# Kernel optimization log

Hardware: AMD Instinct MI355X
Metric: run time of the kernel (lower is better)

## Reference

```python
import jax, jax.numpy as jnp
import numpy as np
from jax import lax

D = 1024      # input_dim
H = 4096      # hidden_dim (4*D)
E = 8         # num_experts
TOPK = 2      # sparse_top_k


def setup_inputs() -> dict:
    key = jax.random.key(0)
    ks = jax.random.split(key, 7)
    s = 0.02
    return {
        "x": jax.random.normal(ks[0], (2, 2048, D), dtype=jnp.float32),
        "W1": jax.random.normal(ks[1], (E, D, H), dtype=jnp.float32) * s,
        "b1": jnp.zeros((E, H), dtype=jnp.float32),
        "W2": jax.random.normal(ks[2], (E, H, D), dtype=jnp.float32) * s,
        "b2": jnp.zeros((E, D), dtype=jnp.float32),
        "Wr": jax.random.normal(ks[3], (D, E), dtype=jnp.float32) * s,
        "br": jnp.zeros((E,), dtype=jnp.float32),
    }


def reference(x, W1, b1, W2, b2, Wr, br):
    B, S, _ = x.shape
    xf = x.reshape(-1, D)                                  # [T, D]
    logits = xf @ Wr + br                                  # [T, E]
    # top-k threshold masking (keep logits >= k-th largest, else -inf)
    topv, _ = lax.top_k(logits, TOPK)                      # [T, k]
    thresh = topv[:, TOPK - 1:TOPK]                        # [T, 1]
    masked = jnp.where(logits >= thresh, logits, -jnp.inf)
    weights = jax.nn.softmax(masked, axis=-1)              # [T, E]
    # run ALL experts densely (faithful to reference), then weighted sum
    h = jax.nn.gelu(jnp.einsum('td,edh->eth', xf, W1) + b1[:, None, :],
                    approximate=False)                     # [E, T, H]
    expert_out = jnp.einsum('eth,ehd->etd', h, W2) + b2[:, None, :]  # [E, T, D]
    out = jnp.einsum('etd,te->td', expert_out, weights)    # [T, D]
    return out.reshape(B, S, D)
```

## Files before the change

### kernel.cpp

```cpp
#include <hip/hip_runtime.h>
#include <math.h>

typedef __bf16 bf16x8 __attribute__((ext_vector_type(8)));
typedef float f32x4 __attribute__((ext_vector_type(4)));

#define DDIM 1024
#define HDIM 4096
#define NE 8
#define TT 4096
#define CAP 9216

static const size_t OFF_CTRL   = 0;
static const size_t OFF_ROWMAP = 256;
static const size_t OFF_WROW   = OFF_ROWMAP + (size_t)CAP * 4;
static const size_t OFF_ROWPOS = OFF_WROW + (size_t)CAP * 4;
static const size_t OFF_TOKE   = OFF_ROWPOS + (size_t)TT * 2 * 4;
static const size_t OFF_TOKW   = OFF_TOKE + (size_t)TT * 2 * 4;
static const size_t OFF_XB     = OFF_TOKW + (size_t)TT * 2 * 4;
static const size_t OFF_W1T    = OFF_XB + (size_t)TT * DDIM * 2;
static const size_t OFF_W2T    = OFF_W1T + (size_t)NE * HDIM * DDIM * 2;
static const size_t OFF_H      = OFF_W2T + (size_t)NE * DDIM * HDIM * 2;
static const size_t OFF_PO     = OFF_H + (size_t)CAP * HDIM * 2;
static const size_t WS_NEED    = OFF_PO + (size_t)CAP * DDIM * 2;

__device__ __forceinline__ unsigned short f2bf(float f) {
  unsigned int u = __builtin_bit_cast(unsigned int, f);
  u = (u + 0x7FFFu + ((u >> 16) & 1u)) >> 16;
  return (unsigned short)u;
}

__device__ __forceinline__ float bf2f(unsigned short s) {
  return __builtin_bit_cast(float, (unsigned int)s << 16);
}

__device__ __forceinline__ void async16(void* lds, const void* g) {
  __builtin_amdgcn_global_load_lds(
      (__attribute__((address_space(1))) void*)g,
      (__attribute__((address_space(3))) void*)lds, 16, 0, 0);
}

__device__ __forceinline__ float gelu_exact(float v) {
  return 0.5f * v * (1.0f + erff(v * 0.70710678118654752f));
}

__global__ __launch_bounds__(256) void router_k(
    const float* __restrict__ x, const float* __restrict__ Wr, const float* __restrict__ br,
    unsigned short* __restrict__ xb, int* __restrict__ toke, float* __restrict__ tokw) {
  int tid = threadIdx.x, lane = tid & 63, wid = tid >> 6;
  int t = blockIdx.x * 4 + wid;
  const float* xr = x + (size_t)t * DDIM;
  float acc[NE];
#pragma unroll
  for (int e = 0; e < NE; ++e) acc[e] = 0.f;
#pragma unroll
  for (int it = 0; it < DDIM / 256; ++it) {
    int d0 = it * 256 + lane * 4;
    float4 xv = *(const float4*)(xr + d0);
    ushort4 xs;
    xs.x = f2bf(xv.x); xs.y = f2bf(xv.y); xs.z = f2bf(xv.z); xs.w = f2bf(xv.w);
    *(ushort4*)(xb + (size_t)t * DDIM + d0) = xs;
    const float4* w0 = (const float4*)(Wr + (size_t)(d0 + 0) * NE);
    const float4* w1 = (const float4*)(Wr + (size_t)(d0 + 1) * NE);
    const float4* w2 = (const float4*)(Wr + (size_t)(d0 + 2) * NE);
    const float4* w3 = (const float4*)(Wr + (size_t)(d0 + 3) * NE);
    float4 a, b;
    a = w0[0]; b = w0[1];
    acc[0] += xv.x * a.x; acc[1] += xv.x * a.y; acc[2] += xv.x * a.z; acc[3] += xv.x * a.w;
    acc[4] += xv.x * b.x; acc[5] += xv.x * b.y; acc[6] += xv.x * b.z; acc[7] += xv.x * b.w;
    a = w1[0]; b = w1[1];
    acc[0] += xv.y * a.x; acc[1] += xv.y * a.y; acc[2] += xv.y * a.z; acc[3] += xv.y * a.w;
    acc[4] += xv.y * b.x; acc[5] += xv.y * b.y; acc[6] += xv.y * b.z; acc[7] += xv.y * b.w;
    a = w2[0]; b = w2[1];
    acc[0] += xv.z * a.x; acc[1] += xv.z * a.y; acc[2] += xv.z * a.z; acc[3] += xv.z * a.w;
    acc[4] += xv.z * b.x; acc[5] += xv.z * b.y; acc[6] += xv.z * b.z; acc[7] += xv.z * b.w;
    a = w3[0]; b = w3[1];
    acc[0] += xv.w * a.x; acc[1] += xv.w * a.y; acc[2] += xv.w * a.z; acc[3] += xv.w * a.w;
    acc[4] += xv.w * b.x; acc[5] += xv.w * b.y; acc[6] += xv.w * b.z; acc[7] += xv.w * b.w;
  }
#pragma unroll
  for (int e = 0; e < NE; ++e) {
#pragma unroll
    for (int s = 32; s > 0; s >>= 1) acc[e] += __shfl_xor(acc[e], s, 64);
  }
  if (lane == 0) {
    float l[NE];
#pragma unroll
    for (int e = 0; e < NE; ++e) l[e] = acc[e] + br[e];
    int i0 = 0; float m0 = l[0];
#pragma unroll
    for (int e = 1; e < NE; ++e) if (l[e] > m0) { m0 = l[e]; i0 = e; }
    int i1 = -1; float m1 = -3.4e38f;
#pragma unroll
    for (int e = 0; e < NE; ++e) if (e != i0 && l[e] > m1) { m1 = l[e]; i1 = e; }
    float e1 = expf(m1 - m0);
    float s = 1.f + e1;
    toke[2 * t] = i0;  toke[2 * t + 1] = i1;
    tokw[2 * t] = 1.f / s;  tokw[2 * t + 1] = e1 / s;
  }
}

__global__ __launch_bounds__(1024) void bin_k(
    const int* __restrict__ toke, const float* __restrict__ tokw,
    int* __restrict__ ctrl, int* __restrict__ rowmap,
    float* __restrict__ wrow, int* __restrict__ rowpos) {
  __shared__ int wcnt[16][8];
  __shared__ int wpre[16][8];
  __shared__ int pbase[9];
  __shared__ int ecnt[8];
  __shared__ int ebase[8];
  int tid = threadIdx.x, lane = tid & 63, w = tid >> 6;

  int myCnt = 0;
  for (int c = 0; c < 8; ++c) {
    int e = toke[c * 1024 + tid];
#pragma unroll
    for (int ee = 0; ee < 8; ++ee) {
      unsigned long long m = __ballot(e == ee);
      if (lane == ee) myCnt += (int)__popcll(m);
    }
  }
  if (lane < 8) wcnt[w][lane] = myCnt;
  __syncthreads();
  if (tid == 0) {
    int off = 0;
    for (int e = 0; e < 8; ++e) {
      int s = 0;
      for (int ww = 0; ww < 16; ++ww) s += wcnt[ww][e];
      ecnt[e] = s;
      pbase[e] = off;
      ebase[e] = off;
      ctrl[8 + e] = off;
      off += ((s + 127) >> 7) << 7;
    }
    pbase[8] = off;
    ctrl[16] = off;
  }
  __syncthreads();

  for (int e = 0; e < 8; ++e) {
    int start = pbase[e] + ecnt[e], end = pbase[e + 1];
    for (int r = start + tid; r < end; r += 1024) { rowmap[r] = 0; wrow[r] = 0.f; }
  }

  for (int c = 0; c < 8; ++c) {
    int slot = c * 1024 + tid;
    int e = toke[slot];
    unsigned long long mown = 0;
#pragma unroll
    for (int ee = 0; ee < 8; ++ee) {
      unsigned long long m = __ballot(e == ee);
      if (lane == ee) wcnt[w][ee] = (int)__popcll(m);
      if (e == ee) mown = m;
    }
    __syncthreads();
    if (tid < 128) {
      int ww = tid >> 3, ee = tid & 7;
      int s = 0;
      for (int p = 0; p < ww; ++p) s += wcnt[p][ee];
      wpre[ww][ee] = s;
    }
    __syncthreads();
    int rank = (int)__popcll(mown & ((1ull << lane) - 1ull));
    int r = ebase[e] + wpre[w][e] + rank;
    rowmap[r] = slot >> 1;
    wrow[r] = tokw[slot];
    rowpos[slot] = r;
    __syncthreads();
    if (tid < 8) {
      int s = 0;
      for (int ww = 0; ww < 16; ++ww) s += wcnt[ww][tid];
      ebase[tid] += s;
    }
    __syncthreads();
  }
}

__global__ __launch_bounds__(256) void convT_k(
    const float* __restrict__ src, unsigned short* __restrict__ dst, int K_, int N_) {
  __shared__ unsigned int lds32[64][33];
  int e = blockIdx.z;
  int kb = blockIdx.y << 6, nb = blockIdx.x << 6;
  int t = threadIdx.x;
  const float* s = src + (size_t)e * K_ * N_ + (size_t)kb * N_ + nb;
  int n0 = (t & 15) << 2;
#pragma unroll
  for (int i = 0; i < 2; ++i) {
    int k2 = (i << 4) + (t >> 4);
    float4 a = *(const float4*)(s + (size_t)(2 * k2) * N_ + n0);
    float4 b = *(const float4*)(s + (size_t)(2 * k2 + 1) * N_ + n0);
    lds32[n0 + 0][k2] = (unsigned)f2bf(a.x) | ((unsigned)f2bf(b.x) << 16);
    lds32[n0 + 1][k2] = (unsigned)f2bf(a.y) | ((unsigned)f2bf(b.y) << 16);
    lds32[n0 + 2][k2] = (unsigned)f2bf(a.z) | ((unsigned)f2bf(b.z) << 16);
    lds32[n0 + 3][k2] = (unsigned)f2bf(a.w) | ((unsigned)f2bf(b.w) << 16);
  }
  __syncthreads();
  unsigned short* dp = dst + (size_t)e * (size_t)N_ * K_ + (size_t)nb * K_ + kb;
  int n = t >> 2, c = t & 3;
  uint4 v0, v1;
  v0.x = lds32[n][(c << 2) + 0]; v0.y = lds32[n][(c << 2) + 1];
  v0.z = lds32[n][(c << 2) + 2]; v0.w = lds32[n][(c << 2) + 3];
  int c4 = (c + 4) << 2;
  v1.x = lds32[n][c4 + 0]; v1.y = lds32[n][c4 + 1];
  v1.z = lds32[n][c4 + 2]; v1.w = lds32[n][c4 + 3];
  *(uint4*)(dp + (size_t)n * K_ + (c << 3)) = v0;
  *(uint4*)(dp + (size_t)n * K_ + ((c + 4) << 3)) = v1;
}

template <int KTOT, int NTOT, bool GATHER, bool DOGELU, bool KSPLIT2>
__global__ __launch_bounds__(256, 2) void gemm_k(
    const unsigned short* __restrict__ A, const unsigned short* __restrict__ Bt,
    const int* __restrict__ ctrl, const int* __restrict__ rowmap,
    const float* __restrict__ wrow, const float* __restrict__ bias,
    unsigned short* __restrict__ out0, unsigned short* __restrict__ out1) {
  __shared__ __align__(16) char SMEM[32768];
  unsigned short* Asm = (unsigned short*)SMEM;
  unsigned short* Bsm = (unsigned short*)(SMEM + 16384);
  int zz = blockIdx.z;
  int e = KSPLIT2 ? (zz & 7) : zz;
  int ks = KSPLIT2 ? (zz >> 3) : 0;
  int off0 = ctrl[8 + e], off1 = ctrl[8 + e + 1];
  int row0 = off0 + (blockIdx.y << 7);
  if (row0 >= off1) return;
  int col0 = blockIdx.x << 7;
  int tid = threadIdx.x, lane = tid & 63, wid = tid >> 6;
  int wr = wid >> 1, wc = wid & 1;
  int kbeg = KSPLIT2 ? ks * (KTOT / 2) : 0;
  int kend = KSPLIT2 ? kbeg + (KTOT / 2) : KTOT;
  unsigned short* outp = (KSPLIT2 && ks) ? out1 : out0;
  if (DOGELU) outp = out0;

  const unsigned short* Asrc[4];
  const unsigned short* Bsrc[4];
#pragma unroll
  for (int c = 0; c < 4; ++c) {
    int ar = row0 + (c << 5) + (tid >> 3);
    size_t arow = GATHER ? (size_t)rowmap[ar] : (size_t)ar;
    Asrc[c] = A + arow * KTOT + ((tid & 7) << 3);
    int brw = col0 + (c << 5) + (tid >> 3);
    Bsrc[c] = Bt + ((size_t)e * NTOT + brw) * KTOT + ((tid & 7) << 3);
  }

  f32x4 acc[4][4];
#pragma unroll
  for (int m = 0; m < 4; ++m)
#pragma unroll
    for (int n = 0; n < 4; ++n) acc[m][n] = (f32x4){0.f, 0.f, 0.f, 0.f};

  int arow_rd = ((wr << 6) + (lane & 15)) << 6;
  int brow_rd = ((wc << 6) + (lane & 15)) << 6;
  int koff = (lane >> 4) << 3;

  for (int k0 = kbeg; k0 < kend; k0 += 64) {
#pragma unroll
    for (int c = 0; c < 4; ++c) {
      async16(SMEM + (((c << 8) + (wid << 6)) << 4), Asrc[c] + k0);
      async16(SMEM + 16384 + (((c << 8) + (wid << 6)) << 4), Bsrc[c] + k0);
    }
    __syncthreads();
#pragma unroll
    for (int kk = 0; kk < 64; kk += 32) {
      bf16x8 af[4], bfr[4];
#pragma unroll
      for (int m = 0; m < 4; ++m)
        af[m] = *(const bf16x8*)&Asm[arow_rd + (m << 10) + kk + koff];
#pragma unroll
      for (int n = 0; n < 4; ++n)
        bfr[n] = *(const bf16x8*)&Bsm[brow_rd + (n << 10) + kk + koff];
#pragma unroll
      for (int m = 0; m < 4; ++m)
#pragma unroll
        for (int n = 0; n < 4; ++n)
          acc[m][n] = __builtin_amdgcn_mfma_f32_16x16x32_bf16(af[m], bfr[n], acc[m][n], 0, 0, 0);
    }
    __syncthreads();
  }

  unsigned short (*Cl)[128] = (unsigned short(*)[128])SMEM;
  int r_b = (lane >> 4) << 2;
  int c_b = lane & 15;
#pragma unroll
  for (int n = 0; n < 4; ++n) {
    int col_l = (wc << 6) + (n << 4) + c_b;
    float bv = (KSPLIT2 && ks) ? 0.f : bias[e * NTOT + col0 + col_l];
#pragma unroll
    for (int m = 0; m < 4; ++m) {
#pragma unroll
      for (int r = 0; r < 4; ++r) {
        int row_l = (wr << 6) + (m << 4) + r_b + r;
        float v = acc[m][n][r] + bv;
        if (DOGELU) {
          Cl[row_l][col_l] = f2bf(gelu_exact(v));
        } else {
          Cl[row_l][col_l] = f2bf(wrow[row0 + row_l] * v);
        }
      }
    }
  }
  __syncthreads();
  int rb = tid >> 4, cof = (tid & 15) << 3;
#pragma unroll
  for (int j = 0; j < 8; ++j) {
    int row_l = rb + (j << 4);
    uint4 v = *(const uint4*)&Cl[row_l][cof];
    *(uint4*)&outp[(size_t)(row0 + row_l) * NTOT + col0 + cof] = v;
  }
}

__global__ __launch_bounds__(256) void gather_k(
    const unsigned short* __restrict__ p0, const unsigned short* __restrict__ p1,
    const int* __restrict__ rowpos, float* __restrict__ out) {
  int t = blockIdx.x, d = threadIdx.x << 2;
  int r0 = rowpos[2 * t], r1 = rowpos[2 * t + 1];
  ushort4 a0 = *(const ushort4*)&p0[(size_t)r0 * DDIM + d];
  ushort4 a1 = *(const ushort4*)&p1[(size_t)r0 * DDIM + d];
  ushort4 b0 = *(const ushort4*)&p0[(size_t)r1 * DDIM + d];
  ushort4 b1 = *(const ushort4*)&p1[(size_t)r1 * DDIM + d];
  float4 o;
  o.x = (bf2f(a0.x) + bf2f(a1.x)) + (bf2f(b0.x) + bf2f(b1.x));
  o.y = (bf2f(a0.y) + bf2f(a1.y)) + (bf2f(b0.y) + bf2f(b1.y));
  o.z = (bf2f(a0.z) + bf2f(a1.z)) + (bf2f(b0.z) + bf2f(b1.z));
  o.w = (bf2f(a0.w) + bf2f(a1.w)) + (bf2f(b0.w) + bf2f(b1.w));
  *(float4*)&out[(size_t)t * DDIM + d] = o;
}

extern "C" void kernel_launch(void* const* d_in, const int* in_sizes, int n_in,
                              void* d_out, int out_size, void* d_ws, size_t ws_size,
                              hipStream_t stream) {
  const float* x  = (const float*)d_in[0];
  const float* W1 = (const float*)d_in[1];
  const float* b1 = (const float*)d_in[2];
  const float* W2 = (const float*)d_in[3];
  const float* b2 = (const float*)d_in[4];
  const float* Wr = (const float*)d_in[5];
  const float* br = (const float*)d_in[6];
  float* out = (float*)d_out;

  if (ws_size < WS_NEED) return;

  char* ws = (char*)d_ws;
  int* ctrl            = (int*)(ws + OFF_CTRL);
  int* rowmap          = (int*)(ws + OFF_ROWMAP);
  float* wrow          = (float*)(ws + OFF_WROW);
  int* rowpos          = (int*)(ws + OFF_ROWPOS);
  int* toke            = (int*)(ws + OFF_TOKE);
  float* tokw          = (float*)(ws + OFF_TOKW);
  unsigned short* xb   = (unsigned short*)(ws + OFF_XB);
  unsigned short* W1T  = (unsigned short*)(ws + OFF_W1T);
  unsigned short* W2T  = (unsigned short*)(ws + OFF_W2T);
  unsigned short* hbuf = (unsigned short*)(ws + OFF_H);
  unsigned short* pout = (unsigned short*)(ws + OFF_PO);
  unsigned short* pout2 = (unsigned short*)(ws + OFF_W1T);

  router_k<<<TT / 4, 256, 0, stream>>>(x, Wr, br, xb, toke, tokw);
  bin_k<<<1, 1024, 0, stream>>>(toke, tokw, ctrl, rowmap, wrow, rowpos);

  convT_k<<<dim3(HDIM / 64, DDIM / 64, NE), 256, 0, stream>>>(W1, W1T, DDIM, HDIM);
  convT_k<<<dim3(DDIM / 64, HDIM / 64, NE), 256, 0, stream>>>(W2, W2T, HDIM, DDIM);

  gemm_k<DDIM, HDIM, true, true, false><<<dim3(HDIM / 128, 32, NE), 256, 0, stream>>>(
      xb, W1T, ctrl, rowmap, wrow, b1, hbuf, nullptr);
  gemm_k<HDIM, DDIM, false, false, true><<<dim3(DDIM / 128, 32, NE * 2), 256, 0, stream>>>(
      hbuf, W2T, ctrl, rowmap, wrow, b2, pout, pout2);

  gather_k<<<TT, 256, 0, stream>>>(pout, pout2, rowpos, out);
}
```

Before: 374.6 us.

## Widen GEMM block tile to 128x256 for more operand reuse

The expert GEMM kernel moves from a 128x128 to a 128x256 output tile per block. Each wave now computes 64x128 with 32 accumulator fragments, and shared memory grows to 48KB to stage the wider B tile. The epilogue is split into four 64-column quarters that go through a smaller LDS staging buffer with extra barriers. The aim is to cut global and LDS traffic per MFMA by reusing A fragments across twice as many columns. The cost is higher register pressure under launch_bounds(256,2), and half as many blocks, which may hurt occupancy and load balance on the many CUs.

```diff
diff --git a/kernel.cpp b/kernel.cpp
--- a/kernel.cpp
+++ b/kernel.cpp
@@ -206,13 +206,13 @@
   *(uint4*)(dp + (size_t)n * K_ + ((c + 4) << 3)) = v1;
 }
 
-template <int KTOT, int NTOT, bool GATHER, bool DOGELU, bool KSPLIT2>
+template <int KTOT, int KLEN, int NTOT, bool GATHER, bool DOGELU, bool KSPLIT2>
 __global__ __launch_bounds__(256, 2) void gemm_k(
     const unsigned short* __restrict__ A, const unsigned short* __restrict__ Bt,
     const int* __restrict__ ctrl, const int* __restrict__ rowmap,
     const float* __restrict__ wrow, const float* __restrict__ bias,
     unsigned short* __restrict__ out0, unsigned short* __restrict__ out1) {
-  __shared__ __align__(16) char SMEM[32768];
+  __shared__ __align__(16) char SMEM[49152];
   unsigned short* Asm = (unsigned short*)SMEM;
   unsigned short* Bsm = (unsigned short*)(SMEM + 16384);
   int zz = blockIdx.z;
@@ -221,88 +221,107 @@
   int off0 = ctrl[8 + e], off1 = ctrl[8 + e + 1];
   int row0 = off0 + (blockIdx.y << 7);
   if (row0 >= off1) return;
-  int col0 = blockIdx.x << 7;
-  int tid = threadIdx.x, lane = tid & 63, wid = tid >> 6;
+  int col0 = blockIdx.x << 8;
+  int tid = threadIdx.x, lane = tid & 63;
+  int wid = tid >> 6;
   int wr = wid >> 1, wc = wid & 1;
-  int kbeg = KSPLIT2 ? ks * (KTOT / 2) : 0;
-  int kend = KSPLIT2 ? kbeg + (KTOT / 2) : KTOT;
+  int kbeg = KSPLIT2 ? ks * KLEN : 0;
   unsigned short* outp = (KSPLIT2 && ks) ? out1 : out0;
   if (DOGELU) outp = out0;
 
   const unsigned short* Asrc[4];
-  const unsigned short* Bsrc[4];
+  const unsigned short* Bsrc[8];
 #pragma unroll
   for (int c = 0; c < 4; ++c) {
     int ar = row0 + (c << 5) + (tid >> 3);
     size_t arow = GATHER ? (size_t)rowmap[ar] : (size_t)ar;
-    Asrc[c] = A + arow * KTOT + ((tid & 7) << 3);
+    Asrc[c] = A + arow * KTOT + kbeg + ((tid & 7) << 3);
+  }
+#pragma unroll
+  for (int c = 0; c < 8; ++c) {
     int brw = col0 + (c << 5) + (tid >> 3);
-    Bsrc[c] = Bt + ((size_t)e * NTOT + brw) * KTOT + ((tid & 7) << 3);
-  }
-
-  f32x4 acc[4][4];
+    Bsrc[c] = Bt + ((size_t)e * NTOT + brw) * KTOT + kbeg + ((tid & 7) << 3);
+  }
+
+  f32x4 acc[4][8];
 #pragma unroll
   for (int m = 0; m < 4; ++m)
 #pragma unroll
-    for (int n = 0; n < 4; ++n) acc[m][n] = (f32x4){0.f, 0.f, 0.f, 0.f};
-
-  int arow_rd = ((wr << 6) + (lane & 15)) << 6;
-  int brow_rd = ((wc << 6) + (lane & 15)) << 6;
+    for (int n = 0; n < 8; ++n) acc[m][n] = (f32x4){0.f, 0.f, 0.f, 0.f};
+
+  int rA[4], rB[8];
+#pragma unroll
+  for (int m = 0; m < 4; ++m) rA[m] = ((wr << 6) + (m << 4) + (lane & 15)) << 6;
+#pragma unroll
+  for (int n = 0; n < 8; ++n) rB[n] = ((wc << 7) + (n << 4) + (lane & 15)) << 6;
   int koff = (lane >> 4) << 3;
 
-  for (int k0 = kbeg; k0 < kend; k0 += 64) {
-#pragma unroll
-    for (int c = 0; c < 4; ++c) {
-      async16(SMEM + (((c << 8) + (wid << 6)) << 4), Asrc[c] + k0);
-      async16(SMEM + 16384 + (((c << 8) + (wid << 6)) << 4), Bsrc[c] + k0);
-    }
+  for (int k0 = 0; k0 < KLEN; k0 += 64) {
+#pragma unroll
+    for (int c = 0; c < 4; ++c)
+      async16(SMEM + c * 4096 + tid * 16, Asrc[c] + k0);
+#pragma unroll
+    for (int c = 0; c < 8; ++c)
+      async16(SMEM + 16384 + c * 4096 + tid * 16, Bsrc[c] + k0);
     __syncthreads();
 #pragma unroll
     for (int kk = 0; kk < 64; kk += 32) {
-      bf16x8 af[4], bfr[4];
+      bf16x8 af[4];
 #pragma unroll
       for (int m = 0; m < 4; ++m)
-        af[m] = *(const bf16x8*)&Asm[arow_rd + (m << 10) + kk + koff];
-#pragma unroll
-      for (int n = 0; n < 4; ++n)
-        bfr[n] = *(const bf16x8*)&Bsm[brow_rd + (n << 10) + kk + koff];
-#pragma unroll
-      for (int m = 0; m < 4; ++m)
+        af[m] = *(const bf16x8*)&Asm[rA[m] + kk + koff];
+#pragma unroll
+      for (int g = 0; g < 2; ++g) {
+        bf16x8 bfr[4];
 #pragma unroll
         for (int n = 0; n < 4; ++n)
-          acc[m][n] = __builtin_amdgcn_mfma_f32_16x16x32_bf16(af[m], bfr[n], acc[m][n], 0, 0, 0);
-    }
-    __syncthreads();
-  }
-
-  unsigned short (*Cl)[128] = (unsigned short(*)[128])SMEM;
+          bfr[n] = *(const bf16x8*)&Bsm[rB[(g << 2) + n] + kk + koff];
+#pragma unroll
+        for (int m = 0; m < 4; ++m)
+#pragma unroll
+          for (int n = 0; n < 4; ++n)
+            acc[m][(g << 2) + n] =
+                __builtin_amdgcn_mfma_f32_16x16x32_bf16(af[m], bfr[n], acc[m][(g << 2) + n], 0, 0, 0);
+      }
+    }
+    __syncthreads();
+  }
+
+  unsigned short (*Cl)[64] = (unsigned short(*)[64])SMEM;
   int r_b = (lane >> 4) << 2;
   int c_b = lane & 15;
 #pragma unroll
-  for (int n = 0; n < 4; ++n) {
-    int col_l = (wc << 6) + (n << 4) + c_b;
-    float bv = (KSPLIT2 && ks) ? 0.f : bias[e * NTOT + col0 + col_l];
-#pragma unroll
-    for (int m = 0; m < 4; ++m) {
-#pragma unroll
-      for (int r = 0; r < 4; ++r) {
-        int row_l = (wr << 6) + (m << 4) + r_b + r;
-        float v = acc[m][n][r] + bv;
-        if (DOGELU) {
-          Cl[row_l][col_l] = f2bf(gelu_exact(v));
-        } else {
-          Cl[row_l][col_l] = f2bf(wrow[row0 + row_l] * v);
+  for (int q = 0; q < 4; ++q) {
+    if (wc == (q >> 1)) {
+#pragma unroll
+      for (int nn = 0; nn < 4; ++nn) {
+        int n = ((q & 1) << 2) + nn;
+        int col_q = (nn << 4) + c_b;
+        float bv = (KSPLIT2 && ks) ? 0.f : bias[e * NTOT + col0 + (q << 6) + col_q];
+#pragma unroll
+        for (int m = 0; m < 4; ++m) {
+#pragma unroll
+          for (int r = 0; r < 4; ++r) {
+            int row_l = (wr << 6) + (m << 4) + r_b + r;
+            float v = acc[m][n][r] + bv;
+            if (DOGELU) {
+              Cl[row_l][col_q] = f2bf(gelu_exact(v));
+            } else {
+              Cl[row_l][col_q] = f2bf(wrow[row0 + row_l] * v);
+            }
+          }
         }
       }
     }
-  }
-  __syncthreads();
-  int rb = tid >> 4, cof = (tid & 15) << 3;
-#pragma unroll
-  for (int j = 0; j < 8; ++j) {
-    int row_l = rb + (j << 4);
-    uint4 v = *(const uint4*)&Cl[row_l][cof];
-    *(uint4*)&outp[(size_t)(row0 + row_l) * NTOT + col0 + cof] = v;
+    __syncthreads();
+    int rb = tid >> 3, cof = (tid & 7) << 3;
+#pragma unroll
+    for (int j = 0; j < 4; ++j) {
+      int row_l = rb + (j << 5);
+      uint4 v = *(const uint4*)&Cl[row_l][cof];
+      *(uint4*)&outp[(size_t)(row0 + row_l) * NTOT + col0 + (q << 6) + cof] = v;
+    }
+    __syncthreads();
   }
 }
 
@@ -357,9 +376,9 @@
   convT_k<<<dim3(HDIM / 64, DDIM / 64, NE), 256, 0, stream>>>(W1, W1T, DDIM, HDIM);
   convT_k<<<dim3(DDIM / 64, HDIM / 64, NE), 256, 0, stream>>>(W2, W2T, HDIM, DDIM);
 
-  gemm_k<DDIM, HDIM, true, true, false><<<dim3(HDIM / 128, 32, NE), 256, 0, stream>>>(
+  gemm_k<DDIM, DDIM, HDIM, true, true, false><<<dim3(HDIM / 256, 32, NE), 256, 0, stream>>>(
       xb, W1T, ctrl, rowmap, wrow, b1, hbuf, nullptr);
-  gemm_k<HDIM, DDIM, false, false, true><<<dim3(DDIM / 128, 32, NE * 2), 256, 0, stream>>>(
+  gemm_k<HDIM, HDIM / 2, DDIM, false, false, true><<<dim3(DDIM / 256, 32, NE * 2), 256, 0, stream>>>(
       hbuf, W2T, ctrl, rowmap, wrow, b2, pout, pout2);
 
   gather_k<<<TT, 256, 0, stream>>>(pout, pout2, rowpos, out);
```

Result: slower. 465.6 us (+24.3%).

## Enlarge GEMM tiles to 256x128 with 512-thread blocks and 8 waves

Applied to the files above, without the earlier changes.

The expert GEMM kernel moves from 128x128 tiles with 4 waves to 256x128 tiles with 8 waves (4 along M, 2 along N). Each B tile loaded into LDS is now reused across twice as many rows, cutting weight traffic per FLOP. The epilogue writes the output in two 128-row halves through LDS, with row clamping and bounds checks for partial tiles, since padding per expert no longer aligns with 256. Risks are more LDS per block (48KB), lower occupancy, and more wasted work on ragged expert segments.

```diff
diff --git a/kernel.cpp b/kernel.cpp
--- a/kernel.cpp
+++ b/kernel.cpp
@@ -206,38 +206,41 @@
   *(uint4*)(dp + (size_t)n * K_ + ((c + 4) << 3)) = v1;
 }
 
-template <int KTOT, int NTOT, bool GATHER, bool DOGELU, bool KSPLIT2>
-__global__ __launch_bounds__(256, 2) void gemm_k(
+template <int KTOT, int KLEN, int NTOT, bool GATHER, bool DOGELU, bool KSPLIT2>
+__global__ __launch_bounds__(512, 2) void gemm_k(
     const unsigned short* __restrict__ A, const unsigned short* __restrict__ Bt,
     const int* __restrict__ ctrl, const int* __restrict__ rowmap,
     const float* __restrict__ wrow, const float* __restrict__ bias,
     unsigned short* __restrict__ out0, unsigned short* __restrict__ out1) {
-  __shared__ __align__(16) char SMEM[32768];
+  __shared__ __align__(16) char SMEM[49152];
   unsigned short* Asm = (unsigned short*)SMEM;
-  unsigned short* Bsm = (unsigned short*)(SMEM + 16384);
+  unsigned short* Bsm = (unsigned short*)(SMEM + 32768);
   int zz = blockIdx.z;
   int e = KSPLIT2 ? (zz & 7) : zz;
   int ks = KSPLIT2 ? (zz >> 3) : 0;
   int off0 = ctrl[8 + e], off1 = ctrl[8 + e + 1];
-  int row0 = off0 + (blockIdx.y << 7);
+  int row0 = off0 + (blockIdx.y << 8);
   if (row0 >= off1) return;
   int col0 = blockIdx.x << 7;
   int tid = threadIdx.x, lane = tid & 63, wid = tid >> 6;
-  int wr = wid >> 1, wc = wid & 1;
-  int kbeg = KSPLIT2 ? ks * (KTOT / 2) : 0;
-  int kend = KSPLIT2 ? kbeg + (KTOT / 2) : KTOT;
+  int wm = wid & 3, wn = wid >> 2;
+  int kbeg = KSPLIT2 ? ks * KLEN : 0;
   unsigned short* outp = (KSPLIT2 && ks) ? out1 : out0;
   if (DOGELU) outp = out0;
 
   const unsigned short* Asrc[4];
-  const unsigned short* Bsrc[4];
+  const unsigned short* Bsrc[2];
 #pragma unroll
   for (int c = 0; c < 4; ++c) {
-    int ar = row0 + (c << 5) + (tid >> 3);
+    int ar = row0 + (c << 6) + (tid >> 3);
+    if (ar > off1 - 1) ar = off1 - 1;
     size_t arow = GATHER ? (size_t)rowmap[ar] : (size_t)ar;
-    Asrc[c] = A + arow * KTOT + ((tid & 7) << 3);
-    int brw = col0 + (c << 5) + (tid >> 3);
-    Bsrc[c] = Bt + ((size_t)e * NTOT + brw) * KTOT + ((tid & 7) << 3);
+    Asrc[c] = A + arow * KTOT + kbeg + ((tid & 7) << 3);
+  }
+#pragma unroll
+  for (int c = 0; c < 2; ++c) {
+    int brw = col0 + (c << 6) + (tid >> 3);
+    Bsrc[c] = Bt + ((size_t)e * NTOT + brw) * KTOT + kbeg + ((tid & 7) << 3);
   }
 
   f32x4 acc[4][4];
@@ -246,26 +249,28 @@
 #pragma unroll
     for (int n = 0; n < 4; ++n) acc[m][n] = (f32x4){0.f, 0.f, 0.f, 0.f};
 
-  int arow_rd = ((wr << 6) + (lane & 15)) << 6;
-  int brow_rd = ((wc << 6) + (lane & 15)) << 6;
+  int rA[4], rB[4];
+#pragma unroll
+  for (int m = 0; m < 4; ++m) rA[m] = ((wm << 6) + (m << 4) + (lane & 15)) << 6;
+#pragma unroll
+  for (int n = 0; n < 4; ++n) rB[n] = ((wn << 6) + (n << 4) + (lane & 15)) << 6;
   int koff = (lane >> 4) << 3;
 
-  for (int k0 = kbeg; k0 < kend; k0 += 64) {
-#pragma unroll
-    for (int c = 0; c < 4; ++c) {
-      async16(SMEM + (((c << 8) + (wid << 6)) << 4), Asrc[c] + k0);
-      async16(SMEM + 16384 + (((c << 8) + (wid << 6)) << 4), Bsrc[c] + k0);
-    }
+  for (int k0 = 0; k0 < KLEN; k0 += 64) {
+#pragma unroll
+    for (int c = 0; c < 4; ++c)
+      async16(SMEM + (c << 13) + (tid << 4), Asrc[c] + k0);
+#pragma unroll
+    for (int c = 0; c < 2; ++c)
+      async16(SMEM + 32768 + (c << 13) + (tid << 4), Bsrc[c] + k0);
     __syncthreads();
 #pragma unroll
     for (int kk = 0; kk < 64; kk += 32) {
       bf16x8 af[4], bfr[4];
 #pragma unroll
-      for (int m = 0; m < 4; ++m)
-        af[m] = *(const bf16x8*)&Asm[arow_rd + (m << 10) + kk + koff];
-#pragma unroll
-      for (int n = 0; n < 4; ++n)
-        bfr[n] = *(const bf16x8*)&Bsm[brow_rd + (n << 10) + kk + koff];
+      for (int m = 0; m < 4; ++m) af[m] = *(const bf16x8*)&Asm[rA[m] + kk + koff];
+#pragma unroll
+      for (int n = 0; n < 4; ++n) bfr[n] = *(const bf16x8*)&Bsm[rB[n] + kk + koff];
 #pragma unroll
       for (int m = 0; m < 4; ++m)
 #pragma unroll
@@ -278,31 +283,46 @@
   unsigned short (*Cl)[128] = (unsigned short(*)[128])SMEM;
   int r_b = (lane >> 4) << 2;
   int c_b = lane & 15;
-#pragma unroll
-  for (int n = 0; n < 4; ++n) {
-    int col_l = (wc << 6) + (n << 4) + c_b;
-    float bv = (KSPLIT2 && ks) ? 0.f : bias[e * NTOT + col0 + col_l];
-#pragma unroll
-    for (int m = 0; m < 4; ++m) {
-#pragma unroll
-      for (int r = 0; r < 4; ++r) {
-        int row_l = (wr << 6) + (m << 4) + r_b + r;
-        float v = acc[m][n][r] + bv;
-        if (DOGELU) {
-          Cl[row_l][col_l] = f2bf(gelu_exact(v));
-        } else {
-          Cl[row_l][col_l] = f2bf(wrow[row0 + row_l] * v);
+  float bv[4];
+#pragma unroll
+  for (int n = 0; n < 4; ++n)
+    bv[n] = (KSPLIT2 && ks) ? 0.f : bias[e * NTOT + col0 + (wn << 6) + (n << 4) + c_b];
+
+#pragma unroll
+  for (int p = 0; p < 2; ++p) {
+    if ((wm >> 1) == p) {
+#pragma unroll
+      for (int n = 0; n < 4; ++n) {
+        int col_l = (wn << 6) + (n << 4) + c_b;
+#pragma unroll
+        for (int m = 0; m < 4; ++m) {
+#pragma unroll
+          for (int r = 0; r < 4; ++r) {
+            int row_l = ((wm & 1) << 6) + (m << 4) + r_b + r;
+            float v = acc[m][n][r] + bv[n];
+            if (DOGELU) {
+              Cl[row_l][col_l] = f2bf(gelu_exact(v));
+            } else {
+              int grow = row0 + (p << 7) + row_l;
+              int rw = grow < off1 ? grow : off0;
+              Cl[row_l][col_l] = f2bf(wrow[rw] * v);
+            }
+          }
         }
       }
     }
-  }
-  __syncthreads();
-  int rb = tid >> 4, cof = (tid & 15) << 3;
-#pragma unroll
-  for (int j = 0; j < 8; ++j) {
-    int row_l = rb + (j << 4);
-    uint4 v = *(const uint4*)&Cl[row_l][cof];
-    *(uint4*)&outp[(size_t)(row0 + row_l) * NTOT + col0 + cof] = v;
+    __syncthreads();
+    int rb = tid >> 4, cof = (tid & 15) << 3;
+#pragma unroll
+    for (int j = 0; j < 4; ++j) {
+      int row_l = rb + (j << 5);
+      int grow = row0 + (p << 7) + row_l;
+      if (grow < off1) {
+        uint4 v = *(const uint4*)&Cl[row_l][cof];
+        *(uint4*)&outp[(size_t)grow * NTOT + col0 + cof] = v;
+      }
+    }
+    __syncthreads();
   }
 }
 
@@ -357,9 +377,11 @@
   convT_k<<<dim3(HDIM / 64, DDIM / 64, NE), 256, 0, stream>>>(W1, W1T, DDIM, HDIM);
   convT_k<<<dim3(DDIM / 64, HDIM / 64, NE), 256, 0, stream>>>(W2, W2T, HDIM, DDIM);
 
-  gemm_k<DDIM, HDIM, true, true, false><<<dim3(HDIM / 128, 32, NE), 256, 0, stream>>>(
+  gemm_k<DDIM, DDIM, HDIM, true, true, false>
+      <<<dim3(HDIM / 128, 16, NE), 512, 0, stream>>>(
       xb, W1T, ctrl, rowmap, wrow, b1, hbuf, nullptr);
-  gemm_k<HDIM, DDIM, false, false, true><<<dim3(DDIM / 128, 32, NE * 2), 256, 0, stream>>>(
+  gemm_k<HDIM, HDIM / 2, DDIM, false, false, true>
+      <<<dim3(DDIM / 128, 16, NE * 2), 512, 0, stream>>>(
       hbuf, W2T, ctrl, rowmap, wrow, b2, pout, pout2);
 
   gather_k<<<TT, 256, 0, stream>>>(pout, pout2, rowpos, out);
```

Result: slower. 438.4 us (+17.0%).

## Co-schedule weight transposes with router and first GEMM in fused launches

Applied to the files above, without the earlier changes.

The W1 fp32-to-bf16 transpose is folded into the router kernel, interleaving eight transpose blocks per router block. The W2 transpose is folded into the first expert GEMM by alternating odd blocks (transpose) and even blocks (GEMM tiles). The aim is to overlap the memory-bound weight conversion with compute-bound GEMM work and to drop separate launches. The cost is heterogeneous blocks within one grid. The 32KB shared allocation applies to the transpose blocks too, which may lower occupancy, and many GEMM blocks exit early, which may leave scheduling uneven.

```diff
diff --git a/kernel.cpp b/kernel.cpp
--- a/kernel.cpp
+++ b/kernel.cpp
@@ -43,11 +43,52 @@
   return 0.5f * v * (1.0f + erff(v * 0.70710678118654752f));
 }
 
-__global__ __launch_bounds__(256) void router_k(
+__device__ __forceinline__ void convT_body(
+    const float* __restrict__ src, unsigned short* __restrict__ dst,
+    int K_, int N_, int e, int kbt, int nbt, char* smem) {
+  unsigned int (*lds32)[33] = (unsigned int(*)[33])smem;
+  int kb = kbt << 6, nb = nbt << 6;
+  int t = threadIdx.x;
+  const float* s = src + (size_t)e * K_ * N_ + (size_t)kb * N_ + nb;
+  int n0 = (t & 15) << 2;
+#pragma unroll
+  for (int i = 0; i < 2; ++i) {
+    int k2 = (i << 4) + (t >> 4);
+    float4 a = *(const float4*)(s + (size_t)(2 * k2) * N_ + n0);
+    float4 b = *(const float4*)(s + (size_t)(2 * k2 + 1) * N_ + n0);
+    lds32[n0 + 0][k2] = (unsigned)f2bf(a.x) | ((unsigned)f2bf(b.x) << 16);
+    lds32[n0 + 1][k2] = (unsigned)f2bf(a.y) | ((unsigned)f2bf(b.y) << 16);
+    lds32[n0 + 2][k2] = (unsigned)f2bf(a.z) | ((unsigned)f2bf(b.z) << 16);
+    lds32[n0 + 3][k2] = (unsigned)f2bf(a.w) | ((unsigned)f2bf(b.w) << 16);
+  }
+  __syncthreads();
+  unsigned short* dp = dst + (size_t)e * (size_t)N_ * K_ + (size_t)nb * K_ + kb;
+  int n = t >> 2, c = t & 3;
+  uint4 v0, v1;
+  v0.x = lds32[n][(c << 2) + 0]; v0.y = lds32[n][(c << 2) + 1];
+  v0.z = lds32[n][(c << 2) + 2]; v0.w = lds32[n][(c << 2) + 3];
+  int c4 = (c + 4) << 2;
+  v1.x = lds32[n][c4 + 0]; v1.y = lds32[n][c4 + 1];
+  v1.z = lds32[n][c4 + 2]; v1.w = lds32[n][c4 + 3];
+  *(uint4*)(dp + (size_t)n * K_ + (c << 3)) = v0;
+  *(uint4*)(dp + (size_t)n * K_ + ((c + 4) << 3)) = v1;
+}
+
+__global__ __launch_bounds__(256) void fat1_k(
     const float* __restrict__ x, const float* __restrict__ Wr, const float* __restrict__ br,
-    unsigned short* __restrict__ xb, int* __restrict__ toke, float* __restrict__ tokw) {
+    unsigned short* __restrict__ xb, int* __restrict__ toke, float* __restrict__ tokw,
+    const float* __restrict__ W1, unsigned short* __restrict__ W1T) {
+  __shared__ __align__(16) char SMEM[8448];
+  int b = blockIdx.x;
+  int g = b / 9, r = b % 9;
+  if (r != 0) {
+    int idx = 8 * g + (r - 1);
+    int e = idx >> 10, rem = idx & 1023;
+    convT_body(W1, W1T, DDIM, HDIM, e, rem >> 6, rem & 63, SMEM);
+    return;
+  }
   int tid = threadIdx.x, lane = tid & 63, wid = tid >> 6;
-  int t = blockIdx.x * 4 + wid;
+  int t = g * 4 + wid;
   const float* xr = x + (size_t)t * DDIM;
   float acc[NE];
 #pragma unroll
@@ -63,19 +104,19 @@
     const float4* w1 = (const float4*)(Wr + (size_t)(d0 + 1) * NE);
     const float4* w2 = (const float4*)(Wr + (size_t)(d0 + 2) * NE);
     const float4* w3 = (const float4*)(Wr + (size_t)(d0 + 3) * NE);
-    float4 a, b;
-    a = w0[0]; b = w0[1];
+    float4 a, bb;
+    a = w0[0]; bb = w0[1];
     acc[0] += xv.x * a.x; acc[1] += xv.x * a.y; acc[2] += xv.x * a.z; acc[3] += xv.x * a.w;
-    acc[4] += xv.x * b.x; acc[5] += xv.x * b.y; acc[6] += xv.x * b.z; acc[7] += xv.x * b.w;
-    a = w1[0]; b = w1[1];
+    acc[4] += xv.x * bb.x; acc[5] += xv.x * bb.y; acc[6] += xv.x * bb.z; acc[7] += xv.x * bb.w;
+    a = w1[0]; bb = w1[1];
     acc[0] += xv.y * a.x; acc[1] += xv.y * a.y; acc[2] += xv.y * a.z; acc[3] += xv.y * a.w;
-    acc[4] += xv.y * b.x; acc[5] += xv.y * b.y; acc[6] += xv.y * b.z; acc[7] += xv.y * b.w;
-    a = w2[0]; b = w2[1];
+    acc[4] += xv.y * bb.x; acc[5] += xv.y * bb.y; acc[6] += xv.y * bb.z; acc[7] += xv.y * bb.w;
+    a = w2[0]; bb = w2[1];
     acc[0] += xv.z * a.x; acc[1] += xv.z * a.y; acc[2] += xv.z * a.z; acc[3] += xv.z * a.w;
-    acc[4] += xv.z * b.x; acc[5] += xv.z * b.y; acc[6] += xv.z * b.z; acc[7] += xv.z * b.w;
-    a = w3[0]; b = w3[1];
+    acc[4] += xv.z * bb.x; acc[5] += xv.z * bb.y; acc[6] += xv.z * bb.z; acc[7] += xv.z * bb.w;
+    a = w3[0]; bb = w3[1];
     acc[0] += xv.w * a.x; acc[1] += xv.w * a.y; acc[2] += xv.w * a.z; acc[3] += xv.w * a.w;
-    acc[4] += xv.w * b.x; acc[5] += xv.w * b.y; acc[6] += xv.w * b.z; acc[7] += xv.w * b.w;
+    acc[4] += xv.w * bb.x; acc[5] += xv.w * bb.y; acc[6] += xv.w * bb.z; acc[7] += xv.w * bb.w;
   }
 #pragma unroll
   for (int e = 0; e < NE; ++e) {
@@ -175,67 +216,128 @@
   }
 }
 
-__global__ __launch_bounds__(256) void convT_k(
-    const float* __restrict__ src, unsigned short* __restrict__ dst, int K_, int N_) {
-  __shared__ unsigned int lds32[64][33];
-  int e = blockIdx.z;
-  int kb = blockIdx.y << 6, nb = blockIdx.x << 6;
-  int t = threadIdx.x;
-  const float* s = src + (size_t)e * K_ * N_ + (size_t)kb * N_ + nb;
-  int n0 = (t & 15) << 2;
-#pragma unroll
-  for (int i = 0; i < 2; ++i) {
-    int k2 = (i << 4) + (t >> 4);
-    float4 a = *(const float4*)(s + (size_t)(2 * k2) * N_ + n0);
-    float4 b = *(const float4*)(s + (size_t)(2 * k2 + 1) * N_ + n0);
-    lds32[n0 + 0][k2] = (unsigned)f2bf(a.x) | ((unsigned)f2bf(b.x) << 16);
-    lds32[n0 + 1][k2] = (unsigned)f2bf(a.y) | ((unsigned)f2bf(b.y) << 16);
-    lds32[n0 + 2][k2] = (unsigned)f2bf(a.z) | ((unsigned)f2bf(b.z) << 16);
-    lds32[n0 + 3][k2] = (unsigned)f2bf(a.w) | ((unsigned)f2bf(b.w) << 16);
-  }
-  __syncthreads();
-  unsigned short* dp = dst + (size_t)e * (size_t)N_ * K_ + (size_t)nb * K_ + kb;
-  int n = t >> 2, c = t & 3;
-  uint4 v0, v1;
-  v0.x = lds32[n][(c << 2) + 0]; v0.y = lds32[n][(c << 2) + 1];
-  v0.z = lds32[n][(c << 2) + 2]; v0.w = lds32[n][(c << 2) + 3];
-  int c4 = (c + 4) << 2;
-  v1.x = lds32[n][c4 + 0]; v1.y = lds32[n][c4 + 1];
-  v1.z = lds32[n][c4 + 2]; v1.w = lds32[n][c4 + 3];
-  *(uint4*)(dp + (size_t)n * K_ + (c << 3)) = v0;
-  *(uint4*)(dp + (size_t)n * K_ + ((c + 4) << 3)) = v1;
-}
-
-template <int KTOT, int NTOT, bool GATHER, bool DOGELU, bool KSPLIT2>
-__global__ __launch_bounds__(256, 2) void gemm_k(
+__global__ __launch_bounds__(256, 2) void fat2_k(
     const unsigned short* __restrict__ A, const unsigned short* __restrict__ Bt,
     const int* __restrict__ ctrl, const int* __restrict__ rowmap,
-    const float* __restrict__ wrow, const float* __restrict__ bias,
+    const float* __restrict__ bias, unsigned short* __restrict__ outb,
+    const float* __restrict__ W2, unsigned short* __restrict__ W2T) {
+  __shared__ __align__(16) char SMEM[32768];
+  int b = blockIdx.x;
+  if (b & 1) {
+    int c = b >> 1;
+    int e = c >> 10, rem = c & 1023;
+    convT_body(W2, W2T, HDIM, DDIM, e, rem >> 4, rem & 15, SMEM);
+    return;
+  }
+  int g = b >> 1;
+  int cx = g & 31, ry = (g >> 5) & 31, e = g >> 10;
+  unsigned short* Asm = (unsigned short*)SMEM;
+  unsigned short* Bsm = (unsigned short*)(SMEM + 16384);
+  int off0 = ctrl[8 + e], off1 = ctrl[8 + e + 1];
+  int row0 = off0 + (ry << 7);
+  if (row0 >= off1) return;
+  int col0 = cx << 7;
+  int tid = threadIdx.x, lane = tid & 63, wid = tid >> 6;
+  int wr = wid >> 1, wc = wid & 1;
+
+  const unsigned short* Asrc[4];
+  const unsigned short* Bsrc[4];
+#pragma unroll
+  for (int c = 0; c < 4; ++c) {
+    int ar = row0 + (c << 5) + (tid >> 3);
+    Asrc[c] = A + (size_t)rowmap[ar] * DDIM + ((tid & 7) << 3);
+    int brw = col0 + (c << 5) + (tid >> 3);
+    Bsrc[c] = Bt + ((size_t)e * HDIM + brw) * DDIM + ((tid & 7) << 3);
+  }
+
+  f32x4 acc[4][4];
+#pragma unroll
+  for (int m = 0; m < 4; ++m)
+#pragma unroll
+    for (int n = 0; n < 4; ++n) acc[m][n] = (f32x4){0.f, 0.f, 0.f, 0.f};
+
+  int arow_rd = ((wr << 6) + (lane & 15)) << 6;
+  int brow_rd = ((wc << 6) + (lane & 15)) << 6;
+  int koff = (lane >> 4) << 3;
+
+  for (int k0 = 0; k0 < DDIM; k0 += 64) {
+#pragma unroll
+    for (int c = 0; c < 4; ++c) {
+      async16(SMEM + (((c << 8) + (wid << 6)) << 4), Asrc[c] + k0);
+      async16(SMEM + 16384 + (((c << 8) + (wid << 6)) << 4), Bsrc[c] + k0);
+    }
+    __syncthreads();
+#pragma unroll
+    for (int kk = 0; kk < 64; kk += 32) {
+      bf16x8 af[4], bfr[4];
+#pragma unroll
+      for (int m = 0; m < 4; ++m)
+        af[m] = *(const bf16x8*)&Asm[arow_rd + (m << 10) + kk + koff];
+#pragma unroll
+      for (int n = 0; n < 4; ++n)
+        bfr[n] = *(const bf16x8*)&Bsm[brow_rd + (n << 10) + kk + koff];
+#pragma unroll
+      for (int m = 0; m < 4; ++m)
+#pragma unroll
+        for (int n = 0; n < 4; ++n)
+          acc[m][n] = __builtin_amdgcn_mfma_f32_16x16x32_bf16(af[m], bfr[n], acc[m][n], 0, 0, 0);
+    }
+    __syncthreads();
+  }
+
+  unsigned short (*Cl)[128] = (unsigned short(*)[128])SMEM;
+  int r_b = (lane >> 4) << 2;
+  int c_b = lane & 15;
+#pragma unroll
+  for (int n = 0; n < 4; ++n) {
+    int col_l = (wc << 6) + (n << 4) + c_b;
+    float bv = bias[e * HDIM + col0 + col_l];
+#pragma unroll
+    for (int m = 0; m < 4; ++m) {
+#pragma unroll
+      for (int r = 0; r < 4; ++r) {
+        int row_l = (wr << 6) + (m << 4) + r_b + r;
+        Cl[row_l][col_l] = f2bf(gelu_exact(acc[m][n][r] + bv));
+      }
+    }
+  }
+  __syncthreads();
+  int rb = tid >> 4, cof = (tid & 15) << 3;
+#pragma unroll
+  for (int j = 0; j < 8; ++j) {
+    int row_l = rb + (j << 4);
+    uint4 v = *(const uint4*)&Cl[row_l][cof];
+    *(uint4*)&outb[(size_t)(row0 + row_l) * HDIM + col0 + cof] = v;
+  }
+}
+
+template <int KTOT, int NTOT>
+__global__ __launch_bounds__(256, 2) void gemm2_k(
+    const unsigned short* __restrict__ A, const unsigned short* __restrict__ Bt,
+    const int* __restrict__ ctrl, const float* __restrict__ wrow,
+    const float* __restrict__ bias,
     unsigned short* __restrict__ out0, unsigned short* __restrict__ out1) {
   __shared__ __align__(16) char SMEM[32768];
   unsigned short* Asm = (unsigned short*)SMEM;
   unsigned short* Bsm = (unsigned short*)(SMEM + 16384);
   int zz = blockIdx.z;
-  int e = KSPLIT2 ? (zz & 7) : zz;
-  int ks = KSPLIT2 ? (zz >> 3) : 0;
+  int e = zz & 7, ks = zz >> 3;
   int off0 = ctrl[8 + e], off1 = ctrl[8 + e + 1];
   int row0 = off0 + (blockIdx.y << 7);
   if (row0 >= off1) return;
   int col0 = blockIdx.x << 7;
   int tid = threadIdx.x, lane = tid & 63, wid = tid >> 6;
   int wr = wid >> 1, wc = wid & 1;
-  int kbeg = KSPLIT2 ? ks * (KTOT / 2) : 0;
-  int kend = KSPLIT2 ? kbeg + (KTOT / 2) : KTOT;
-  unsigned short* outp = (KSPLIT2 && ks) ? out1 : out0;
-  if (DOGELU) outp = out0;
+  int kbeg = ks * (KTOT / 2);
+  int kend = kbeg + (KTOT / 2);
+  unsigned short* outp = ks ? out1 : out0;
 
   const unsigned short* Asrc[4];
   const unsigned short* Bsrc[4];
 #pragma unroll
   for (int c = 0; c < 4; ++c) {
     int ar = row0 + (c << 5) + (tid >> 3);
-    size_t arow = GATHER ? (size_t)rowmap[ar] : (size_t)ar;
-    Asrc[c] = A + arow * KTOT + ((tid & 7) << 3);
+    Asrc[c] = A + (size_t)ar * KTOT + ((tid & 7) << 3);
     int brw = col0 + (c << 5) + (tid >> 3);
     Bsrc[c] = Bt + ((size_t)e * NTOT + brw) * KTOT + ((tid & 7) << 3);
   }
@@ -281,18 +383,13 @@
 #pragma unroll
   for (int n = 0; n < 4; ++n) {
     int col_l = (wc << 6) + (n << 4) + c_b;
-    float bv = (KSPLIT2 && ks) ? 0.f : bias[e * NTOT + col0 + col_l];
+    float bv = ks ? 0.f : bias[e * NTOT + col0 + col_l];
 #pragma unroll
     for (int m = 0; m < 4; ++m) {
 #pragma unroll
       for (int r = 0; r < 4; ++r) {
         int row_l = (wr << 6) + (m << 4) + r_b + r;
-        float v = acc[m][n][r] + bv;
-        if (DOGELU) {
-          Cl[row_l][col_l] = f2bf(gelu_exact(v));
-        } else {
-          Cl[row_l][col_l] = f2bf(wrow[row0 + row_l] * v);
-        }
+        Cl[row_l][col_l] = f2bf(wrow[row0 + row_l] * (acc[m][n][r] + bv));
       }
     }
   }
@@ -351,16 +448,13 @@
   unsigned short* pout = (unsigned short*)(ws + OFF_PO);
   unsigned short* pout2 = (unsigned short*)(ws + OFF_W1T);
 
-  router_k<<<TT / 4, 256, 0, stream>>>(x, Wr, br, xb, toke, tokw);
+  fat1_k<<<9216, 256, 0, stream>>>(x, Wr, br, xb, toke, tokw, W1, W1T);
   bin_k<<<1, 1024, 0, stream>>>(toke, tokw, ctrl, rowmap, wrow, rowpos);
 
-  convT_k<<<dim3(HDIM / 64, DDIM / 64, NE), 256, 0, stream>>>(W1, W1T, DDIM, HDIM);
-  convT_k<<<dim3(DDIM / 64, HDIM / 64, NE), 256, 0, stream>>>(W2, W2T, HDIM, DDIM);
-
-  gemm_k<DDIM, HDIM, true, true, false><<<dim3(HDIM / 128, 32, NE), 256, 0, stream>>>(
-      xb, W1T, ctrl, rowmap, wrow, b1, hbuf, nullptr);
-  gemm_k<HDIM, DDIM, false, false, true><<<dim3(DDIM / 128, 32, NE * 2), 256, 0, stream>>>(
-      hbuf, W2T, ctrl, rowmap, wrow, b2, pout, pout2);
+  fat2_k<<<16384, 256, 0, stream>>>(xb, W1T, ctrl, rowmap, b1, hbuf, W2, W2T);
+
+  gemm2_k<HDIM, DDIM><<<dim3(DDIM / 128, 32, NE * 2), 256, 0, stream>>>(
+      hbuf, W2T, ctrl, wrow, b2, pout, pout2);
 
   gather_k<<<TT, 256, 0, stream>>>(pout, pout2, rowpos, out);
 }
```

Result: slower. 408.3 us (+9.0%).
